# Performance work log

Hardware: AMD Instinct MI355X
Metric: run time of the kernel (lower is better)

## Reference

```python
import jax, jax.numpy as jnp
import numpy as np
import math

H = 16
D_MODEL = 1024
D_K = 64
BS = 8
SEQ = 1024


def setup_inputs() -> dict:
    key = jax.random.key(0)
    ks = jax.random.split(key, 13)
    s = 1.0 / math.sqrt(D_MODEL)
    inp = {
        "q": jax.random.normal(ks[0], (BS, SEQ, D_MODEL), dtype=jnp.float32),
        "k": jax.random.normal(ks[1], (BS, SEQ, D_MODEL), dtype=jnp.float32),
        "v": jax.random.normal(ks[2], (BS, SEQ, D_MODEL), dtype=jnp.float32),
        "mask": jax.random.randint(ks[3], (BS, SEQ, SEQ), 0, 2, dtype=jnp.int32),
        "Wq": jax.random.normal(ks[4], (D_MODEL, D_MODEL), dtype=jnp.float32) * s,
        "bq": jax.random.normal(ks[5], (D_MODEL,), dtype=jnp.float32) * s,
        "Wk": jax.random.normal(ks[6], (D_MODEL, D_MODEL), dtype=jnp.float32) * s,
        "bk": jax.random.normal(ks[7], (D_MODEL,), dtype=jnp.float32) * s,
        "Wv": jax.random.normal(ks[8], (D_MODEL, D_MODEL), dtype=jnp.float32) * s,
        "bv": jax.random.normal(ks[9], (D_MODEL,), dtype=jnp.float32) * s,
        "Wo": jax.random.normal(ks[10], (D_MODEL, D_MODEL), dtype=jnp.float32) * s,
        "bo": jax.random.normal(ks[11], (D_MODEL,), dtype=jnp.float32) * s,
    }
    return inp


def reference(q, k, v, mask, Wq, bq, Wk, bk, Wv, bv, Wo, bo):
    bs, seq, _ = q.shape
    # projections, split heads: [b, h, s, dk]
    def proj(x, W, b):
        y = x @ W + b
        return y.reshape(bs, seq, H, D_K).transpose(0, 2, 1, 3)
    qh = proj(q, Wq, bq)
    kh = proj(k, Wk, bk)
    vh = proj(v, Wv, bv)
    # scaled dot-product attention (dropout is identity in eval mode)
    scores = jnp.einsum("bhqd,bhkd->bhqk", qh, kh) / math.sqrt(D_K)
    scores = jnp.where(mask[:, None, :, :] == 0, jnp.float32(-1e9), scores)
    attn = jax.nn.softmax(scores, axis=-1)
    ctx = jnp.einsum("bhqk,bhkd->bhqd", attn, vh)
    concat = ctx.transpose(0, 2, 1, 3).reshape(bs, seq, D_MODEL)
    return concat @ Wo + bo
```

## Files before the change

kernel.cpp:

```cpp
#include <hip/hip_runtime.h>
#include <hip/hip_bf16.h>

#define HN 16
#define DM 1024
#define DK 64
#define BSZ 8
#define SEQL 1024

typedef __attribute__((ext_vector_type(8))) short bf16x8;
typedef __attribute__((ext_vector_type(4))) short short4v;
typedef __attribute__((ext_vector_type(4))) float f32x4;

__device__ __forceinline__ short f2bf(float f) {
    union { float f; unsigned u; } x; x.f = f;
    unsigned u = x.u + 0x7FFFu + ((x.u >> 16) & 1u);
    return (short)(u >> 16);
}

__device__ __forceinline__ void async16(const short* g, short* ldsbase) {
    __builtin_amdgcn_global_load_lds(
        (const __attribute__((address_space(1))) unsigned int*)g,
        (__attribute__((address_space(3))) unsigned int*)ldsbase, 16, 0, 0);
}

__device__ __forceinline__ short4v pack4bf(float v0, float v1, float v2, float v3) {
    unsigned pk0, pk1;
    asm("v_cvt_pk_bf16_f32 %0, %1, %2" : "=v"(pk0) : "v"(v0), "v"(v1));
    asm("v_cvt_pk_bf16_f32 %0, %1, %2" : "=v"(pk1) : "v"(v2), "v"(v3));
    union { unsigned u[2]; short4v s4; } u_;
    u_.u[0] = pk0; u_.u[1] = pk1;
    return u_.s4;
}

__global__ __launch_bounds__(256) void cast_bf16(const float* __restrict__ in,
                                                 short* __restrict__ out) {
    size_t i = (size_t)blockIdx.x * 256 + threadIdx.x;
    float4 a = ((const float4*)in)[2 * i];
    float4 b = ((const float4*)in)[2 * i + 1];
    bf16x8 r = {f2bf(a.x), f2bf(a.y), f2bf(a.z), f2bf(a.w),
                f2bf(b.x), f2bf(b.y), f2bf(b.z), f2bf(b.w)};
    ((bf16x8*)out)[i] = r;
}

__global__ __launch_bounds__(256) void transpose_cast(const float* __restrict__ W,
                                                      short* __restrict__ Wt) {
    __shared__ float tile[32][33];
    const int t = threadIdx.x;
    const int k0 = blockIdx.x * 32, n0 = blockIdx.y * 32;
    const int c = t & 31, r = t >> 5;
    #pragma unroll
    for (int p = 0; p < 4; ++p)
        tile[r + 8 * p][c] = W[(size_t)(k0 + r + 8 * p) * DM + n0 + c];
    __syncthreads();
    #pragma unroll
    for (int p = 0; p < 4; ++p)
        Wt[(size_t)(n0 + r + 8 * p) * DM + k0 + c] = f2bf(tile[c][r + 8 * p]);
}

__global__ __launch_bounds__(256) void pack_mask(const int* __restrict__ mask,
                                                 unsigned short* __restrict__ bt) {
    size_t gi = (size_t)blockIdx.x * 256 + threadIdx.x;
    size_t word = gi >> 6;
    int l = threadIdx.x & 63;
    int jperm = ((l >> 2) & 3) * 16 + ((l >> 4) & 3) * 4 + (l & 3);
    size_t row = word >> 4;
    int jblk = (int)(word & 15);
    unsigned long long b = __ballot(mask[row * SEQL + jblk * 64 + jperm] != 0);
    if (l < 4)
        bt[row * 64 + l * 16 + jblk] = (unsigned short)(b >> (l * 16));
}

template <int MODE>
__global__ __launch_bounds__(256) void gemm_mfma(const short* __restrict__ A,
                                                 const short* __restrict__ Wt,
                                                 const float* __restrict__ bias,
                                                 void* __restrict__ Cp) {
    __shared__ __attribute__((aligned(16))) short As[2][128][32];
    __shared__ __attribute__((aligned(16))) short Bs[2][128][32];
    const int t = threadIdx.x;
    const int lane = t & 63, wv = t >> 6;
    const int wm = (wv >> 1) * 64, wn = (wv & 1) * 64;
    const int quad = lane >> 4, l15 = lane & 15;
    const int tileM = blockIdx.x * 128, tileN = blockIdx.y * 128;
    const size_t zoff = (size_t)blockIdx.z * DM * SEQL;
    const short* Az = A + zoff;

    const int sr = wv * 16 + (lane >> 2);
    const int sc = (lane & 3) * 8;
    const short* asrc = Az + (size_t)(tileM + sr) * DM + sc;
    const short* bsrc = Wt + (size_t)(tileN + sr) * DM + sc;

    f32x4 acc[4][4];
    #pragma unroll
    for (int i = 0; i < 4; ++i)
        #pragma unroll
        for (int j = 0; j < 4; ++j) acc[i][j] = {0.f, 0.f, 0.f, 0.f};

    #pragma unroll
    for (int p = 0; p < 2; ++p) {
        async16(asrc + (size_t)p * 64 * DM, &As[0][p * 64 + wv * 16][0]);
        async16(bsrc + (size_t)p * 64 * DM, &Bs[0][p * 64 + wv * 16][0]);
    }
    __syncthreads();

    #pragma unroll 2
    for (int idx = 0; idx < DM / 32; ++idx) {
        const int cur = idx & 1;
        const int k0 = idx * 32;
        if (k0 + 32 < DM) {
            #pragma unroll
            for (int p = 0; p < 2; ++p) {
                async16(asrc + (size_t)p * 64 * DM + (k0 + 32),
                        &As[cur ^ 1][p * 64 + wv * 16][0]);
                async16(bsrc + (size_t)p * 64 * DM + (k0 + 32),
                        &Bs[cur ^ 1][p * 64 + wv * 16][0]);
            }
        }

        bf16x8 a[4], b[4];
        #pragma unroll
        for (int i = 0; i < 4; ++i) a[i] = *(const bf16x8*)&As[cur][wm + i * 16 + l15][quad * 8];
        #pragma unroll
        for (int j = 0; j < 4; ++j) b[j] = *(const bf16x8*)&Bs[cur][wn + j * 16 + l15][quad * 8];
        #pragma unroll
        for (int i = 0; i < 4; ++i)
            #pragma unroll
            for (int j = 0; j < 4; ++j)
                acc[i][j] = __builtin_amdgcn_mfma_f32_16x16x32_bf16(a[i], b[j], acc[i][j], 0, 0, 0);

        __syncthreads();
    }

    if (MODE == 2) {
        short* C = (short*)Cp + zoff;
        #pragma unroll
        for (int i = 0; i < 4; ++i)
            #pragma unroll
            for (int j = 0; j < 4; ++j) {
                int rowb = tileM + wm + i * 16 + quad * 4;
                int col = tileN + wn + j * 16 + l15;
                float b = bias[col];
                short4v s4 = pack4bf(acc[i][j][0] + b, acc[i][j][1] + b,
                                     acc[i][j][2] + b, acc[i][j][3] + b);
                *(short4v*)(C + (size_t)col * SEQL + rowb) = s4;
            }
    } else {
        #pragma unroll
        for (int i = 0; i < 4; ++i)
            #pragma unroll
            for (int j = 0; j < 4; ++j)
                #pragma unroll
                for (int rr = 0; rr < 4; ++rr) {
                    int row = tileM + wm + i * 16 + quad * 4 + rr;
                    int col = tileN + wn + j * 16 + l15;
                    float v = acc[i][j][rr] + bias[col];
                    if (MODE == 0) {
                        short* C = (short*)Cp + zoff;
                        C[((size_t)(col >> 6) * SEQL + row) * DK + (col & 63)] = f2bf(v);
                    } else {
                        float* C = (float*)Cp + zoff;
                        C[(size_t)row * DM + col] = v;
                    }
                }
    }
}

template <bool USE_BITS>
__global__ __launch_bounds__(256) void attn_mfma(const short* __restrict__ Qw,
                                                 const short* __restrict__ Kw,
                                                 const short* __restrict__ Vt,
                                                 const void* __restrict__ maskp,
                                                 short* __restrict__ ctx) {
    __shared__ __attribute__((aligned(16))) short Kbuf[2][64 * 64];
    __shared__ __attribute__((aligned(16))) short Vbuf[2][64 * 64];
    __shared__ __attribute__((aligned(16))) short Ps[4][16 * 64];
    const int t = threadIdx.x;
    const int lane = t & 63, w = t >> 6;
    const int quad = lane >> 4, l15 = lane & 15;
    const int nwg = gridDim.x;
    const int cpx = nwg >> 3;
    const int vb = (blockIdx.x & 7) * cpx + (blockIdx.x >> 3);
    const int q0 = (vb & 15) * 64;
    const int h = (vb >> 4) & 15;
    const int z = vb >> 8;
    const size_t zoff = (size_t)z * DM * SEQL;
    const short* Qb = Qw + zoff + (size_t)h * SEQL * DK;
    const short* Kb = Kw + zoff + (size_t)h * SEQL * DK;
    const short* Vb = Vt + zoff + (size_t)h * DK * SEQL;
    const int qrow = q0 + w * 16 + l15;
    const int x = (l15 & 7) << 3;

    bf16x8 qf0 = *(const bf16x8*)(Qb + (size_t)qrow * DK + quad * 8);
    bf16x8 qf1 = *(const bf16x8*)(Qb + (size_t)qrow * DK + 32 + quad * 8);

    unsigned long long mA = 0, mB = 0, mC = 0, mD = 0;
    if (USE_BITS) {
        const unsigned long long* bt64 = (const unsigned long long*)
            ((const unsigned short*)maskp + (size_t)z * SEQL * 64 +
             (size_t)qrow * 64 + quad * 16);
        mA = bt64[0]; mB = bt64[1]; mC = bt64[2]; mD = bt64[3];
    }

    const int r0 = t >> 3;
    const int kc = ((t & 7) ^ (r0 & 7)) * 8;
    const short* ks0 = Kb + (size_t)r0 * DK + kc;
    const short* ks1 = ks0 + 32 * DK;
    const short* vs0 = Vb + (size_t)r0 * SEQL + kc;
    const short* vs1 = vs0 + 32 * SEQL;

    async16(ks0, &Kbuf[0][w * 512]);
    async16(ks1, &Kbuf[0][2048 + w * 512]);
    async16(vs0, &Vbuf[0][w * 512]);
    async16(vs1, &Vbuf[0][2048 + w * 512]);
    ks0 += 64 * DK; ks1 += 64 * DK; vs0 += 64; vs1 += 64;
    __syncthreads();

    f32x4 o[4];
    #pragma unroll
    for (int td = 0; td < 4; ++td) o[td] = {0.f, 0.f, 0.f, 0.f};
    float Lacc = 0.f;

    #pragma unroll 2
    for (int iter = 0; iter < 16; ++iter) {
        const int cur = iter & 1;
        if (iter < 15) {
            async16(ks0, &Kbuf[cur ^ 1][w * 512]);
            async16(ks1, &Kbuf[cur ^ 1][2048 + w * 512]);
            async16(vs0, &Vbuf[cur ^ 1][w * 512]);
            async16(vs1, &Vbuf[cur ^ 1][2048 + w * 512]);
            ks0 += 64 * DK; ks1 += 64 * DK; vs0 += 64; vs1 += 64;
        }

        const short* Kl = &Kbuf[cur][0];
        const short* Vl = &Vbuf[cur][0];
        unsigned mw16 = 0;
        if (USE_BITS) {
            unsigned long long t01 = (iter & 4) ? mB : mA;
            unsigned long long t23 = (iter & 4) ? mD : mC;
            unsigned long long tw = (iter & 8) ? t23 : t01;
            mw16 = (unsigned)(tw >> ((iter & 3) * 16)) & 0xFFFFu;
        }

        #pragma unroll
        for (int tn = 0; tn < 4; ++tn) {
            const int r = tn * 16 + l15;
            bf16x8 ak0 = *(const bf16x8*)&Kl[r * 64 + ((quad * 8) ^ x)];
            bf16x8 ak1 = *(const bf16x8*)&Kl[r * 64 + ((32 + quad * 8) ^ x)];
            f32x4 s = {0.f, 0.f, 0.f, 0.f};
            s = __builtin_amdgcn_mfma_f32_16x16x32_bf16(ak0, qf0, s, 0, 0, 0);
            s = __builtin_amdgcn_mfma_f32_16x16x32_bf16(ak1, qf1, s, 0, 0, 0);
            float pv[4];
            const unsigned nib = USE_BITS ? (mw16 >> (tn * 4)) & 0xFu : 0u;
            #pragma unroll
            for (int rr = 0; rr < 4; ++rr) {
                bool keep;
                if (USE_BITS) {
                    keep = (nib >> rr) & 1u;
                } else {
                    const int* mi = (const int*)maskp + (size_t)z * SEQL * SEQL;
                    keep = mi[(size_t)qrow * SEQL + iter * 64 + tn * 16 + quad * 4 + rr] != 0;
                }
                float e = __expf(s[rr] * 0.125f);
                pv[rr] = keep ? e : 0.0f;
                Lacc += pv[rr];
            }
            *(short4v*)&Ps[w][l15 * 64 + ((tn * 16 + quad * 4) ^ x)] =
                pack4bf(pv[0], pv[1], pv[2], pv[3]);
        }
        bf16x8 ap0 = *(const bf16x8*)&Ps[w][l15 * 64 + ((quad * 8) ^ x)];
        bf16x8 ap1 = *(const bf16x8*)&Ps[w][l15 * 64 + ((32 + quad * 8) ^ x)];
        #pragma unroll
        for (int td = 0; td < 4; ++td) {
            const int r = td * 16 + l15;
            bf16x8 bv0 = *(const bf16x8*)&Vl[r * 64 + ((quad * 8) ^ x)];
            bf16x8 bv1 = *(const bf16x8*)&Vl[r * 64 + ((32 + quad * 8) ^ x)];
            o[td] = __builtin_amdgcn_mfma_f32_16x16x32_bf16(ap0, bv0, o[td], 0, 0, 0);
            o[td] = __builtin_amdgcn_mfma_f32_16x16x32_bf16(ap1, bv1, o[td], 0, 0, 0);
        }

        __syncthreads();
    }

    Lacc += __shfl_xor(Lacc, 16);
    Lacc += __shfl_xor(Lacc, 32);
    float Linv = 1.0f / Lacc;
    float Linv4[4];
    #pragma unroll
    for (int rr = 0; rr < 4; ++rr)
        Linv4[rr] = __shfl(Linv, quad * 4 + rr);

    short* cb = ctx + zoff;
    #pragma unroll
    for (int td = 0; td < 4; ++td)
        #pragma unroll
        for (int rr = 0; rr < 4; ++rr) {
            int rq = q0 + w * 16 + quad * 4 + rr;
            int cd = h * 64 + td * 16 + l15;
            cb[(size_t)rq * DM + cd] = f2bf(o[td][rr] * Linv4[rr]);
        }
}

extern "C" void kernel_launch(void* const* d_in, const int* in_sizes, int n_in,
                              void* d_out, int out_size, void* d_ws, size_t ws_size,
                              hipStream_t stream) {
    const float* q  = (const float*)d_in[0];
    const float* k  = (const float*)d_in[1];
    const float* v  = (const float*)d_in[2];
    const int* mask = (const int*)d_in[3];
    const float* Wq = (const float*)d_in[4];
    const float* bq = (const float*)d_in[5];
    const float* Wk = (const float*)d_in[6];
    const float* bk = (const float*)d_in[7];
    const float* Wv = (const float*)d_in[8];
    const float* bv = (const float*)d_in[9];
    const float* Wo = (const float*)d_in[10];
    const float* bo = (const float*)d_in[11];
    float* out = (float*)d_out;

    const size_t MB = (size_t)1 << 20;
    const size_t MEL = (size_t)1024 * 1024;
    char* base = (char*)d_ws;

    short* Wqt = (short*)(base + 0 * 2 * MB);
    short* Wkt = (short*)(base + 1 * 2 * MB);
    short* Wvt = (short*)(base + 2 * 2 * MB);
    short* Wot = (short*)(base + 3 * 2 * MB);

    int zdim;
    bool use_bits;
    if      (ws_size >= 74 * MB) { zdim = 8; use_bits = true; }
    else if (ws_size >= 42 * MB) { zdim = 4; use_bits = true; }
    else if (ws_size >= 26 * MB) { zdim = 2; use_bits = true; }
    else if (ws_size >= 18 * MB) { zdim = 1; use_bits = true; }
    else                         { zdim = 1; use_bits = false; }

    unsigned short* bits = (unsigned short*)(base + 8 * MB);
    char* bufs = base + (use_bits ? 9 : 8) * MB;
    const size_t bufB = (size_t)zdim * 2 * MB;
    short* Qw  = (short*)(bufs);
    short* Kw  = (short*)(bufs + bufB);
    short* Vw  = (short*)(bufs + 2 * bufB);
    short* ctx = (short*)(bufs + 3 * bufB);

    transpose_cast<<<dim3(32, 32), 256, 0, stream>>>(Wq, Wqt);
    transpose_cast<<<dim3(32, 32), 256, 0, stream>>>(Wk, Wkt);
    transpose_cast<<<dim3(32, 32), 256, 0, stream>>>(Wv, Wvt);
    transpose_cast<<<dim3(32, 32), 256, 0, stream>>>(Wo, Wot);
    if (use_bits)
        pack_mask<<<(BSZ * SEQL * SEQL) / 256, 256, 0, stream>>>(mask, bits);

    const int iters = BSZ / zdim;
    for (int it = 0; it < iters; ++it) {
        const size_t boff = (size_t)it * zdim * MEL;
        const float* qb = q + boff;
        const float* kb = k + boff;
        const float* vb = v + boff;
        float* ob = out + boff;
        const void* mb = use_bits
            ? (const void*)(bits + (size_t)it * zdim * SEQL * 64)
            : (const void*)(mask + (size_t)it * zdim * SEQL * SEQL);

        const int castGrid = zdim * 512;
        cast_bf16<<<castGrid, 256, 0, stream>>>(qb, ctx);
        gemm_mfma<0><<<dim3(8, 8, zdim), 256, 0, stream>>>(ctx, Wqt, bq, Qw);
        cast_bf16<<<castGrid, 256, 0, stream>>>(kb, ctx);
        gemm_mfma<0><<<dim3(8, 8, zdim), 256, 0, stream>>>(ctx, Wkt, bk, Kw);
        cast_bf16<<<castGrid, 256, 0, stream>>>(vb, ctx);
        gemm_mfma<2><<<dim3(8, 8, zdim), 256, 0, stream>>>(ctx, Wvt, bv, Vw);

        const int attnBlocks = 16 * 16 * zdim;
        if (use_bits)
            attn_mfma<true><<<attnBlocks, 256, 0, stream>>>(Qw, Kw, Vw, mb, ctx);
        else
            attn_mfma<false><<<attnBlocks, 256, 0, stream>>>(Qw, Kw, Vw, mb, ctx);

        gemm_mfma<1><<<dim3(8, 8, zdim), 256, 0, stream>>>(ctx, Wot, bo, ob);
    }
}
```

Baseline: 379.0 us.

## Fuse fp32-to-bf16 cast into a single batched QKV projection GEMM

Removes the separate cast_bf16 kernels. The new gemm_qkv loads the fp32 activations straight into LDS through an XOR swizzle and converts them to bf16 in registers before the MFMA, and it runs the Q, K and V projections in one launch over a 3x z-grid. The four weight transposes are also merged into one launch, and s_setprio hints are wrapped around the MFMA sections in the attention kernel. This cuts kernel launches and the round trip of the bf16 activation copy through global memory, and raises parallelism per launch. In exchange, fp32 tiles double the LDS traffic for A and the conversion is repeated by every N-tile.

```diff
diff --git a/kernel.cpp b/kernel.cpp
--- a/kernel.cpp
+++ b/kernel.cpp
@@ -17,7 +17,7 @@
     return (short)(u >> 16);
 }
 
-__device__ __forceinline__ void async16(const short* g, short* ldsbase) {
+__device__ __forceinline__ void async16(const void* g, void* ldsbase) {
     __builtin_amdgcn_global_load_lds(
         (const __attribute__((address_space(1))) unsigned int*)g,
         (__attribute__((address_space(3))) unsigned int*)ldsbase, 16, 0, 0);
@@ -32,19 +32,25 @@
     return u_.s4;
 }
 
-__global__ __launch_bounds__(256) void cast_bf16(const float* __restrict__ in,
-                                                 short* __restrict__ out) {
-    size_t i = (size_t)blockIdx.x * 256 + threadIdx.x;
-    float4 a = ((const float4*)in)[2 * i];
-    float4 b = ((const float4*)in)[2 * i + 1];
-    bf16x8 r = {f2bf(a.x), f2bf(a.y), f2bf(a.z), f2bf(a.w),
-                f2bf(b.x), f2bf(b.y), f2bf(b.z), f2bf(b.w)};
-    ((bf16x8*)out)[i] = r;
-}
-
-__global__ __launch_bounds__(256) void transpose_cast(const float* __restrict__ W,
-                                                      short* __restrict__ Wt) {
+__device__ __forceinline__ bf16x8 pack8bf(f32x4 lo, f32x4 hi) {
+    union { short4v h[2]; bf16x8 v; } u_;
+    u_.h[0] = pack4bf(lo.x, lo.y, lo.z, lo.w);
+    u_.h[1] = pack4bf(hi.x, hi.y, hi.z, hi.w);
+    return u_.v;
+}
+
+__global__ __launch_bounds__(256) void transpose_cast4(const float* __restrict__ W0,
+                                                       const float* __restrict__ W1,
+                                                       const float* __restrict__ W2,
+                                                       const float* __restrict__ W3,
+                                                       short* __restrict__ T0,
+                                                       short* __restrict__ T1,
+                                                       short* __restrict__ T2,
+                                                       short* __restrict__ T3) {
     __shared__ float tile[32][33];
+    const int zi = blockIdx.z;
+    const float* W = zi == 0 ? W0 : zi == 1 ? W1 : zi == 2 ? W2 : W3;
+    short* Wt = zi == 0 ? T0 : zi == 1 ? T1 : zi == 2 ? T2 : T3;
     const int t = threadIdx.x;
     const int k0 = blockIdx.x * 32, n0 = blockIdx.y * 32;
     const int c = t & 31, r = t >> 5;
@@ -70,11 +76,118 @@
         bt[row * 64 + l * 16 + jblk] = (unsigned short)(b >> (l * 16));
 }
 
-template <int MODE>
-__global__ __launch_bounds__(256) void gemm_mfma(const short* __restrict__ A,
-                                                 const short* __restrict__ Wt,
-                                                 const float* __restrict__ bias,
-                                                 void* __restrict__ Cp) {
+__global__ __launch_bounds__(256) void gemm_qkv(
+    const float* __restrict__ Aq, const float* __restrict__ Ak,
+    const float* __restrict__ Av,
+    const short* __restrict__ Wqt, const short* __restrict__ Wkt,
+    const short* __restrict__ Wvt,
+    const float* __restrict__ bqp, const float* __restrict__ bkp,
+    const float* __restrict__ bvp,
+    short* __restrict__ Cq, short* __restrict__ Ck, short* __restrict__ Cv,
+    int zlog) {
+    __shared__ __attribute__((aligned(16))) float Af[2][128][32];
+    __shared__ __attribute__((aligned(16))) short Bs[2][128][32];
+    const int t = threadIdx.x;
+    const int lane = t & 63, wv = t >> 6;
+    const int wm = (wv >> 1) * 64, wn = (wv & 1) * 64;
+    const int quad = lane >> 4, l15 = lane & 15;
+    const int tileM = blockIdx.x * 128, tileN = blockIdx.y * 128;
+    const int which = blockIdx.z >> zlog;
+    const int zz = blockIdx.z & ((1 << zlog) - 1);
+    const size_t zoff = (size_t)zz * DM * SEQL;
+    const float* A = (which == 0 ? Aq : which == 1 ? Ak : Av) + zoff;
+    const short* Wt = which == 0 ? Wqt : which == 1 ? Wkt : Wvt;
+    const float* bias = which == 0 ? bqp : which == 1 ? bkp : bvp;
+    short* C = (which == 0 ? Cq : which == 1 ? Ck : Cv) + zoff;
+
+    const int arow = t >> 3;
+    const int acol = ((t & 7) ^ (arow & 7)) * 4;
+    const float* asrc = A + (size_t)(tileM + arow) * DM + acol;
+    const int brow = t >> 2;
+    const int bcol = (t & 3) * 8;
+    const short* bsrc = Wt + (size_t)(tileN + brow) * DM + bcol;
+
+    f32x4 acc[4][4];
+    #pragma unroll
+    for (int i = 0; i < 4; ++i)
+        #pragma unroll
+        for (int j = 0; j < 4; ++j) acc[i][j] = {0.f, 0.f, 0.f, 0.f};
+
+    #pragma unroll
+    for (int p = 0; p < 4; ++p)
+        async16(asrc + (size_t)(p * 32) * DM, &Af[0][p * 32 + wv * 8][0]);
+    #pragma unroll
+    for (int p = 0; p < 2; ++p)
+        async16(bsrc + (size_t)(p * 64) * DM, &Bs[0][p * 64 + wv * 16][0]);
+    __syncthreads();
+
+    #pragma unroll 2
+    for (int idx = 0; idx < DM / 32; ++idx) {
+        const int cur = idx & 1;
+        const int k0 = idx * 32;
+        if (k0 + 32 < DM) {
+            #pragma unroll
+            for (int p = 0; p < 4; ++p)
+                async16(asrc + (size_t)(p * 32) * DM + (k0 + 32),
+                        &Af[cur ^ 1][p * 32 + wv * 8][0]);
+            #pragma unroll
+            for (int p = 0; p < 2; ++p)
+                async16(bsrc + (size_t)(p * 64) * DM + (k0 + 32),
+                        &Bs[cur ^ 1][p * 64 + wv * 16][0]);
+        }
+
+        bf16x8 a[4], b[4];
+        #pragma unroll
+        for (int i = 0; i < 4; ++i) {
+            const int r = wm + i * 16 + l15;
+            const int s = r & 7;
+            f32x4 lo = *(const f32x4*)&Af[cur][r][((2 * quad) ^ s) * 4];
+            f32x4 hi = *(const f32x4*)&Af[cur][r][((2 * quad + 1) ^ s) * 4];
+            a[i] = pack8bf(lo, hi);
+        }
+        #pragma unroll
+        for (int j = 0; j < 4; ++j)
+            b[j] = *(const bf16x8*)&Bs[cur][wn + j * 16 + l15][quad * 8];
+        #pragma unroll
+        for (int i = 0; i < 4; ++i)
+            #pragma unroll
+            for (int j = 0; j < 4; ++j)
+                acc[i][j] = __builtin_amdgcn_mfma_f32_16x16x32_bf16(a[i], b[j], acc[i][j], 0, 0, 0);
+
+        __syncthreads();
+    }
+
+    if (which == 2) {
+        #pragma unroll
+        for (int i = 0; i < 4; ++i)
+            #pragma unroll
+            for (int j = 0; j < 4; ++j) {
+                int rowb = tileM + wm + i * 16 + quad * 4;
+                int col = tileN + wn + j * 16 + l15;
+                float bb = bias[col];
+                short4v s4 = pack4bf(acc[i][j][0] + bb, acc[i][j][1] + bb,
+                                     acc[i][j][2] + bb, acc[i][j][3] + bb);
+                *(short4v*)(C + (size_t)col * SEQL + rowb) = s4;
+            }
+    } else {
+        #pragma unroll
+        for (int i = 0; i < 4; ++i)
+            #pragma unroll
+            for (int j = 0; j < 4; ++j)
+                #pragma unroll
+                for (int rr = 0; rr < 4; ++rr) {
+                    int row = tileM + wm + i * 16 + quad * 4 + rr;
+                    int col = tileN + wn + j * 16 + l15;
+                    float v = acc[i][j][rr] + bias[col];
+                    C[((size_t)(col >> 6) * SEQL + row) * DK + (col & 63)] = f2bf(v);
+                }
+    }
+}
+
+__global__ __launch_bounds__(256) void gemm_out(const short* __restrict__ A,
+                                                const short* __restrict__ Wt,
+                                                const float* __restrict__ bias,
+                                                float* __restrict__ Cp) {
     __shared__ __attribute__((aligned(16))) short As[2][128][32];
     __shared__ __attribute__((aligned(16))) short Bs[2][128][32];
     const int t = threadIdx.x;
@@ -131,38 +244,17 @@
         __syncthreads();
     }
 
-    if (MODE == 2) {
-        short* C = (short*)Cp + zoff;
-        #pragma unroll
-        for (int i = 0; i < 4; ++i)
-            #pragma unroll
-            for (int j = 0; j < 4; ++j) {
-                int rowb = tileM + wm + i * 16 + quad * 4;
+    float* C = Cp + zoff;
+    #pragma unroll
+    for (int i = 0; i < 4; ++i)
+        #pragma unroll
+        for (int j = 0; j < 4; ++j)
+            #pragma unroll
+            for (int rr = 0; rr < 4; ++rr) {
+                int row = tileM + wm + i * 16 + quad * 4 + rr;
                 int col = tileN + wn + j * 16 + l15;
-                float b = bias[col];
-                short4v s4 = pack4bf(acc[i][j][0] + b, acc[i][j][1] + b,
-                                     acc[i][j][2] + b, acc[i][j][3] + b);
-                *(short4v*)(C + (size_t)col * SEQL + rowb) = s4;
+                C[(size_t)row * DM + col] = acc[i][j][rr] + bias[col];
             }
-    } else {
-        #pragma unroll
-        for (int i = 0; i < 4; ++i)
-            #pragma unroll
-            for (int j = 0; j < 4; ++j)
-                #pragma unroll
-                for (int rr = 0; rr < 4; ++rr) {
-                    int row = tileM + wm + i * 16 + quad * 4 + rr;
-                    int col = tileN + wn + j * 16 + l15;
-                    float v = acc[i][j][rr] + bias[col];
-                    if (MODE == 0) {
-                        short* C = (short*)Cp + zoff;
-                        C[((size_t)(col >> 6) * SEQL + row) * DK + (col & 63)] = f2bf(v);
-                    } else {
-                        float* C = (float*)Cp + zoff;
-                        C[(size_t)row * DM + col] = v;
-                    }
-                }
-    }
 }
 
 template <bool USE_BITS>
@@ -247,8 +339,10 @@
             bf16x8 ak0 = *(const bf16x8*)&Kl[r * 64 + ((quad * 8) ^ x)];
             bf16x8 ak1 = *(const bf16x8*)&Kl[r * 64 + ((32 + quad * 8) ^ x)];
             f32x4 s = {0.f, 0.f, 0.f, 0.f};
+            __builtin_amdgcn_s_setprio(1);
             s = __builtin_amdgcn_mfma_f32_16x16x32_bf16(ak0, qf0, s, 0, 0, 0);
             s = __builtin_amdgcn_mfma_f32_16x16x32_bf16(ak1, qf1, s, 0, 0, 0);
+            __builtin_amdgcn_s_setprio(0);
             float pv[4];
             const unsigned nib = USE_BITS ? (mw16 >> (tn * 4)) & 0xFu : 0u;
             #pragma unroll
@@ -269,6 +363,7 @@
         }
         bf16x8 ap0 = *(const bf16x8*)&Ps[w][l15 * 64 + ((quad * 8) ^ x)];
         bf16x8 ap1 = *(const bf16x8*)&Ps[w][l15 * 64 + ((32 + quad * 8) ^ x)];
+        __builtin_amdgcn_s_setprio(1);
         #pragma unroll
         for (int td = 0; td < 4; ++td) {
             const int r = td * 16 + l15;
@@ -277,6 +372,7 @@
             o[td] = __builtin_amdgcn_mfma_f32_16x16x32_bf16(ap0, bv0, o[td], 0, 0, 0);
             o[td] = __builtin_amdgcn_mfma_f32_16x16x32_bf16(ap1, bv1, o[td], 0, 0, 0);
         }
+        __builtin_amdgcn_s_setprio(0);
 
         __syncthreads();
     }
@@ -333,6 +429,7 @@
     else if (ws_size >= 26 * MB) { zdim = 2; use_bits = true; }
     else if (ws_size >= 18 * MB) { zdim = 1; use_bits = true; }
     else                         { zdim = 1; use_bits = false; }
+    const int zlog = (zdim == 8) ? 3 : (zdim == 4) ? 2 : (zdim == 2) ? 1 : 0;
 
     unsigned short* bits = (unsigned short*)(base + 8 * MB);
     char* bufs = base + (use_bits ? 9 : 8) * MB;
@@ -342,10 +439,8 @@
     short* Vw  = (short*)(bufs + 2 * bufB);
     short* ctx = (short*)(bufs + 3 * bufB);
 
-    transpose_cast<<<dim3(32, 32), 256, 0, stream>>>(Wq, Wqt);
-    transpose_cast<<<dim3(32, 32), 256, 0, stream>>>(Wk, Wkt);
-    transpose_cast<<<dim3(32, 32), 256, 0, stream>>>(Wv, Wvt);
-    transpose_cast<<<dim3(32, 32), 256, 0, stream>>>(Wo, Wot);
+    transpose_cast4<<<dim3(32, 32, 4), 256, 0, stream>>>(Wq, Wk, Wv, Wo,
+                                                         Wqt, Wkt, Wvt, Wot);
     if (use_bits)
         pack_mask<<<(BSZ * SEQL * SEQL) / 256, 256, 0, stream>>>(mask, bits);
 
@@ -360,13 +455,8 @@
             ? (const void*)(bits + (size_t)it * zdim * SEQL * 64)
             : (const void*)(mask + (size_t)it * zdim * SEQL * SEQL);
 
-        const int castGrid = zdim * 512;
-        cast_bf16<<<castGrid, 256, 0, stream>>>(qb, ctx);
-        gemm_mfma<0><<<dim3(8, 8, zdim), 256, 0, stream>>>(ctx, Wqt, bq, Qw);
-        cast_bf16<<<castGrid, 256, 0, stream>>>(kb, ctx);
-        gemm_mfma<0><<<dim3(8, 8, zdim), 256, 0, stream>>>(ctx, Wkt, bk, Kw);
-        cast_bf16<<<castGrid, 256, 0, stream>>>(vb, ctx);
-        gemm_mfma<2><<<dim3(8, 8, zdim), 256, 0, stream>>>(ctx, Wvt, bv, Vw);
+        gemm_qkv<<<dim3(8, 8, 3 * zdim), 256, 0, stream>>>(
+            qb, kb, vb, Wqt, Wkt, Wvt, bq, bk, bv, Qw, Kw, Vw, zlog);
 
         const int attnBlocks = 16 * 16 * zdim;
         if (use_bits)
@@ -374,6 +464,6 @@
         else
             attn_mfma<false><<<attnBlocks, 256, 0, stream>>>(Qw, Kw, Vw, mb, ctx);
 
-        gemm_mfma<1><<<dim3(8, 8, zdim), 256, 0, stream>>>(ctx, Wot, bo, ob);
-    }
-}
+        gemm_out<<<dim3(8, 8, zdim), 256, 0, stream>>>(ctx, Wot, bo, ob);
+    }
+}
```

Result: slower. 395.5 us (+4.4%).
